# Optimization experiments

Measured on AMD Instinct MI355X. Metric: run time of the kernel, lower is better.

Reference implementation:

```python
import jax, jax.numpy as jnp
import numpy as np


def setup_inputs() -> dict:
    key = jax.random.key(0)
    k1, k2 = jax.random.split(key)
    B, N = 2, 8192
    pred = jax.random.normal(k1, (B, N, 3), dtype=jnp.float32)
    gt = jax.random.normal(k2, (B, N, 3), dtype=jnp.float32)
    return {"pred": pred, "gt": gt}


def reference(pred, gt):
    # dist[b, i, j] = ||pred[b, j] - gt[b, i]||_2, computed via the
    # squared-norm expansion to avoid materializing a [B,N,N,3] diff tensor.
    p_sq = jnp.sum(pred * pred, axis=-1)  # [B, N]
    g_sq = jnp.sum(gt * gt, axis=-1)      # [B, N]
    # inner[b, i, j] = gt[b, i] . pred[b, j]
    inner = jnp.einsum("bid,bjd->bij", gt, pred)  # [B, N, N]
    sq_dist = g_sq[:, :, None] + p_sq[:, None, :] - 2.0 * inner
    dist = jnp.sqrt(jnp.maximum(sq_dist, 0.0))    # [B, N, N]
    dist1 = jnp.min(dist, axis=2)  # per-gt nearest pred distance, [B, N]
    dist2 = jnp.min(dist, axis=1)  # per-pred nearest gt distance, [B, N]
    chamfer = (dist1.mean(axis=1) + dist2.mean(axis=1)).mean()
    return chamfer
```

## Files before the change

kernel.cpp:

```cpp
#include <hip/hip_runtime.h>
#include <math.h>

#define NPTS   8192
#define BATCH  2
#define TPB    256
#define PPB    32
#define NBLK   (2 * BATCH * NPTS / PPB)
#define CHUNK  2048
#define NCHUNK (NPTS / CHUNK)
#define NSL    64
#define GPS    (CHUNK / NSL / 4)
#define SPAD   (GPS + 1)
#define KPT    (PPB / 4)
#define POISON 0xAAAAAAAAu
#define TARGET (POISON + (unsigned)NBLK - 1u)
#define SCALE  (1.0f / (float)(BATCH * NPTS))

typedef float v2f __attribute__((ext_vector_type(2)));
typedef float v4f __attribute__((ext_vector_type(4)));

__global__ __launch_bounds__(TPB, 4) void chamfer_fused(
    const float* __restrict__ pred, const float* __restrict__ gt,
    unsigned int* __restrict__ ws, float* __restrict__ out)
{
    __shared__ v4f xs4[NSL * SPAD], ys4[NSL * SPAD], zs4[NSL * SPAD], qs4[NSL * SPAD];
    __shared__ float psq_l[PPB];

    const int tid = threadIdx.x;
    const int pg  = tid & 3;
    const int cs  = tid >> 2;

    const int base = blockIdx.x * PPB;
    const int dir  = base >> 14;
    const int b    = (base >> 13) & 1;
    const int i0   = base & (NPTS - 1);

    const float* pts  = (dir == 0 ? gt : pred) + (size_t)b * NPTS * 3;
    const float* cand = (dir == 0 ? pred : gt) + (size_t)b * NPTS * 3;

    float px[KPT], py[KPT], pz[KPT], m[KPT];
    {
        float pc[24];
        const v4f* p4 = (const v4f*)(pts + (size_t)(i0 + pg * KPT) * 3);
#pragma unroll
        for (int j = 0; j < 6; ++j) {
            v4f t = p4[j];
            pc[4*j+0] = t.x; pc[4*j+1] = t.y; pc[4*j+2] = t.z; pc[4*j+3] = t.w;
        }
#pragma unroll
        for (int k = 0; k < KPT; ++k) {
            px[k] = pc[3*k]; py[k] = pc[3*k+1]; pz[k] = pc[3*k+2];
            m[k] = 3.0e38f;
        }
    }

    const v4f* cand4 = (const v4f*)cand;
    for (int c = 0; c < NCHUNK; ++c) {
        if (c) __syncthreads();
#pragma unroll
        for (int r = 0; r < 2; ++r) {
            int n = r * TPB + tid;
            v4f a  = cand4[(size_t)c * (CHUNK * 3 / 4) + n * 3 + 0];
            v4f bb = cand4[(size_t)c * (CHUNK * 3 / 4) + n * 3 + 1];
            v4f cc = cand4[(size_t)c * (CHUNK * 3 / 4) + n * 3 + 2];
            v4f X = {a.x, a.w, bb.z, cc.y};
            v4f Y = {a.y, bb.x, bb.w, cc.z};
            v4f Z = {a.z, bb.y, cc.x, cc.w};
            v4f Q = 0.5f * (X * X + Y * Y + Z * Z);
            int idx = (n >> 3) * SPAD + (n & 7);
            xs4[idx] = X; ys4[idx] = Y; zs4[idx] = Z; qs4[idx] = Q;
        }
        __syncthreads();

#pragma unroll
        for (int g = 0; g < GPS; ++g) {
            int idx = cs * SPAD + g;
            v4f cx = xs4[idx], cy = ys4[idx], cz = zs4[idx], cq = qs4[idx];
            v2f cxa = cx.xy, cxb = cx.zw, cya = cy.xy, cyb = cy.zw;
            v2f cza = cz.xy, czb = cz.zw, cqa = cq.xy, cqb = cq.zw;
#pragma unroll
            for (int k = 0; k < KPT; ++k) {
                v2f ta = cqa - cxa * px[k];
                ta = ta - cya * py[k];
                ta = ta - cza * pz[k];
                v2f tb = cqb - cxb * px[k];
                tb = tb - cyb * py[k];
                tb = tb - czb * pz[k];
                m[k] = fminf(fminf(m[k], ta.x), ta.y);
                m[k] = fminf(fminf(m[k], tb.x), tb.y);
            }
        }
    }

    __syncthreads();
    float* pl = (float*)xs4;
#pragma unroll
    for (int k = 0; k < KPT; ++k)
        pl[(pg * KPT + k) * 68 + cs] = m[k];
    if (cs == 0) {
#pragma unroll
        for (int k = 0; k < KPT; ++k)
            psq_l[pg * KPT + k] = fmaf(px[k], px[k], fmaf(py[k], py[k], pz[k] * pz[k]));
    }
    __syncthreads();

    if (tid < PPB) {
        const v4f* pm4 = (const v4f*)pl;
        v4f mv = pm4[tid * 17];
#pragma unroll
        for (int j = 1; j < 16; ++j) {
            v4f t = pm4[tid * 17 + j];
            mv.x = fminf(mv.x, t.x); mv.y = fminf(mv.y, t.y);
            mv.z = fminf(mv.z, t.z); mv.w = fminf(mv.w, t.w);
        }
        float M = fminf(fminf(mv.x, mv.y), fminf(mv.z, mv.w));
        float d = sqrtf(fmaxf(fmaf(2.0f, M, psq_l[tid]), 0.0f));
#pragma unroll
        for (int off = 16; off > 0; off >>= 1) d += __shfl_down(d, off, 32);

        float* accum = (float*)ws;
        unsigned int* counter = ws + 2048;
        int last = 0;
        if (tid == 0) {
            atomicAdd(&accum[(blockIdx.x & 31) * 32], d * SCALE);
            __threadfence();
            unsigned int old = atomicAdd(counter, 1u);
            last = (old == TARGET) ? 1 : 0;
        }
        last = __shfl(last, 0, 32);
        if (last) {
            __threadfence();
            float s = atomicAdd(&accum[tid * 32], 0.0f);
#pragma unroll
            for (int off = 16; off > 0; off >>= 1) s += __shfl_down(s, off, 32);
            if (tid == 0) out[0] = s;
        }
    }
}

extern "C" void kernel_launch(void* const* d_in, const int* in_sizes, int n_in,
                              void* d_out, int out_size, void* d_ws, size_t ws_size,
                              hipStream_t stream) {
    const float* pred = (const float*)d_in[0];
    const float* gt   = (const float*)d_in[1];
    chamfer_fused<<<NBLK, TPB, 0, stream>>>(pred, gt, (unsigned int*)d_ws,
                                            (float*)d_out);
}
```

Before: 92.91 us.

## Prefetch next candidate chunk into registers while computing current chunk

The loop now issues the global loads for the next 2048-point candidate chunk into registers before computing on the current chunk held in shared memory, then writes them to LDS after a barrier. Within a chunk, the next group of LDS vectors is loaded one step ahead of its use. The aim is to hide global and LDS load latency behind the FMA/min work. In exchange, each thread holds 24 more live floats, which raises register pressure and may affect occupancy at launch_bounds(256,4).

```diff
diff --git a/kernel.cpp b/kernel.cpp
--- a/kernel.cpp
+++ b/kernel.cpp
@@ -40,55 +40,90 @@
 
     float px[KPT], py[KPT], pz[KPT], m[KPT];
     {
-        float pc[24];
         const v4f* p4 = (const v4f*)(pts + (size_t)(i0 + pg * KPT) * 3);
+        v4f A0 = p4[0], A1 = p4[1], A2 = p4[2], A3 = p4[3], A4 = p4[4], A5 = p4[5];
+        px[0] = A0.x; py[0] = A0.y; pz[0] = A0.z;
+        px[1] = A0.w; py[1] = A1.x; pz[1] = A1.y;
+        px[2] = A1.z; py[2] = A1.w; pz[2] = A2.x;
+        px[3] = A2.y; py[3] = A2.z; pz[3] = A2.w;
+        px[4] = A3.x; py[4] = A3.y; pz[4] = A3.z;
+        px[5] = A3.w; py[5] = A4.x; pz[5] = A4.y;
+        px[6] = A4.z; py[6] = A4.w; pz[6] = A5.x;
+        px[7] = A5.y; py[7] = A5.z; pz[7] = A5.w;
 #pragma unroll
-        for (int j = 0; j < 6; ++j) {
-            v4f t = p4[j];
-            pc[4*j+0] = t.x; pc[4*j+1] = t.y; pc[4*j+2] = t.z; pc[4*j+3] = t.w;
-        }
-#pragma unroll
-        for (int k = 0; k < KPT; ++k) {
-            px[k] = pc[3*k]; py[k] = pc[3*k+1]; pz[k] = pc[3*k+2];
-            m[k] = 3.0e38f;
-        }
+        for (int k = 0; k < KPT; ++k) m[k] = 3.0e38f;
     }
 
     const v4f* cand4 = (const v4f*)cand;
+
+    {
+        v4f a0 = cand4[tid * 3 + 0];
+        v4f b0 = cand4[tid * 3 + 1];
+        v4f c0 = cand4[tid * 3 + 2];
+        v4f a1 = cand4[(TPB + tid) * 3 + 0];
+        v4f b1 = cand4[(TPB + tid) * 3 + 1];
+        v4f c1 = cand4[(TPB + tid) * 3 + 2];
+        int n0 = tid, n1 = TPB + tid;
+        v4f X0 = {a0.x, a0.w, b0.z, c0.y}, Y0 = {a0.y, b0.x, b0.w, c0.z};
+        v4f Z0 = {a0.z, b0.y, c0.x, c0.w}, Q0 = 0.5f * (X0*X0 + Y0*Y0 + Z0*Z0);
+        v4f X1 = {a1.x, a1.w, b1.z, c1.y}, Y1 = {a1.y, b1.x, b1.w, c1.z};
+        v4f Z1 = {a1.z, b1.y, c1.x, c1.w}, Q1 = 0.5f * (X1*X1 + Y1*Y1 + Z1*Z1);
+        int i0s = (n0 >> 3) * SPAD + (n0 & 7), i1s = (n1 >> 3) * SPAD + (n1 & 7);
+        xs4[i0s] = X0; ys4[i0s] = Y0; zs4[i0s] = Z0; qs4[i0s] = Q0;
+        xs4[i1s] = X1; ys4[i1s] = Y1; zs4[i1s] = Z1; qs4[i1s] = Q1;
+    }
+    __syncthreads();
+
     for (int c = 0; c < NCHUNK; ++c) {
-        if (c) __syncthreads();
+        v4f s0, s1, s2, s3, s4, s5;
+        if (c + 1 < NCHUNK) {
+            const v4f* cb = cand4 + (size_t)(c + 1) * (CHUNK * 3 / 4);
+            s0 = cb[tid * 3 + 0];
+            s1 = cb[tid * 3 + 1];
+            s2 = cb[tid * 3 + 2];
+            s3 = cb[(TPB + tid) * 3 + 0];
+            s4 = cb[(TPB + tid) * 3 + 1];
+            s5 = cb[(TPB + tid) * 3 + 2];
+        }
+
+        {
+            const int ib = cs * SPAD;
+            v4f cxA = xs4[ib], cyA = ys4[ib], czA = zs4[ib], cqA = qs4[ib];
 #pragma unroll
-        for (int r = 0; r < 2; ++r) {
-            int n = r * TPB + tid;
-            v4f a  = cand4[(size_t)c * (CHUNK * 3 / 4) + n * 3 + 0];
-            v4f bb = cand4[(size_t)c * (CHUNK * 3 / 4) + n * 3 + 1];
-            v4f cc = cand4[(size_t)c * (CHUNK * 3 / 4) + n * 3 + 2];
-            v4f X = {a.x, a.w, bb.z, cc.y};
-            v4f Y = {a.y, bb.x, bb.w, cc.z};
-            v4f Z = {a.z, bb.y, cc.x, cc.w};
-            v4f Q = 0.5f * (X * X + Y * Y + Z * Z);
-            int idx = (n >> 3) * SPAD + (n & 7);
-            xs4[idx] = X; ys4[idx] = Y; zs4[idx] = Z; qs4[idx] = Q;
+            for (int g = 0; g < GPS; ++g) {
+                v4f cxB, cyB, czB, cqB;
+                if (g + 1 < GPS) {
+                    cxB = xs4[ib + g + 1]; cyB = ys4[ib + g + 1];
+                    czB = zs4[ib + g + 1]; cqB = qs4[ib + g + 1];
+                }
+                v2f cxa = cxA.xy, cxb = cxA.zw, cya = cyA.xy, cyb = cyA.zw;
+                v2f cza = czA.xy, czb = czA.zw, cqa = cqA.xy, cqb = cqA.zw;
+#pragma unroll
+                for (int k = 0; k < KPT; ++k) {
+                    v2f ta = cqa - cxa * px[k];
+                    ta = ta - cya * py[k];
+                    ta = ta - cza * pz[k];
+                    v2f tb = cqb - cxb * px[k];
+                    tb = tb - cyb * py[k];
+                    tb = tb - czb * pz[k];
+                    m[k] = fminf(fminf(m[k], ta.x), ta.y);
+                    m[k] = fminf(fminf(m[k], tb.x), tb.y);
+                }
+                if (g + 1 < GPS) { cxA = cxB; cyA = cyB; czA = czB; cqA = cqB; }
+            }
         }
-        __syncthreads();
 
-#pragma unroll
-        for (int g = 0; g < GPS; ++g) {
-            int idx = cs * SPAD + g;
-            v4f cx = xs4[idx], cy = ys4[idx], cz = zs4[idx], cq = qs4[idx];
-            v2f cxa = cx.xy, cxb = cx.zw, cya = cy.xy, cyb = cy.zw;
-            v2f cza = cz.xy, czb = cz.zw, cqa = cq.xy, cqb = cq.zw;
-#pragma unroll
-            for (int k = 0; k < KPT; ++k) {
-                v2f ta = cqa - cxa * px[k];
-                ta = ta - cya * py[k];
-                ta = ta - cza * pz[k];
-                v2f tb = cqb - cxb * px[k];
-                tb = tb - cyb * py[k];
-                tb = tb - czb * pz[k];
-                m[k] = fminf(fminf(m[k], ta.x), ta.y);
-                m[k] = fminf(fminf(m[k], tb.x), tb.y);
-            }
+        if (c + 1 < NCHUNK) {
+            __syncthreads();
+            int n0 = tid, n1 = TPB + tid;
+            v4f X0 = {s0.x, s0.w, s1.z, s2.y}, Y0 = {s0.y, s1.x, s1.w, s2.z};
+            v4f Z0 = {s0.z, s1.y, s2.x, s2.w}, Q0 = 0.5f * (X0*X0 + Y0*Y0 + Z0*Z0);
+            v4f X1 = {s3.x, s3.w, s4.z, s5.y}, Y1 = {s3.y, s4.x, s4.w, s5.z};
+            v4f Z1 = {s3.z, s4.y, s5.x, s5.w}, Q1 = 0.5f * (X1*X1 + Y1*Y1 + Z1*Z1);
+            int i0s = (n0 >> 3) * SPAD + (n0 & 7), i1s = (n1 >> 3) * SPAD + (n1 & 7);
+            xs4[i0s] = X0; ys4[i0s] = Y0; zs4[i0s] = Z0; qs4[i0s] = Q0;
+            xs4[i1s] = X1; ys4[i1s] = Y1; zs4[i1s] = Z1; qs4[i1s] = Q1;
+            __syncthreads();
         }
     }
 
```

After: 246.8 us. +165.6%, slower.
